# Performance work log

Measured on AMD Instinct MI355X. Metric: run time of the kernel, lower is better.

Reference implementation:

```python
import jax, jax.numpy as jnp
import numpy as np
import math

B, NX, NY = 8, 1024, 1024
DIM_X = DIM_Y = DIM = 1024
H = 8


def layer_norm(x, g, b, eps=1e-5):
    mu = jnp.mean(x, axis=-1, keepdims=True)
    var = jnp.mean(jnp.square(x - mu), axis=-1, keepdims=True)
    return (x - mu) * jax.lax.rsqrt(var + eps) * g + b


def setup_inputs() -> dict:
    key = jax.random.key(0)
    ks = jax.random.split(key, 12)
    s = 1.0 / math.sqrt(DIM)
    return {
        "X": jax.random.normal(ks[0], (B, NX, DIM_X), jnp.float32),
        "Y": jax.random.normal(ks[1], (B, NY, DIM_Y), jnp.float32),
        "mask": jax.random.bernoulli(ks[2], 0.1, (B, NY)),  # True = masked out
        "Wq": jax.random.normal(ks[3], (DIM_X, DIM), jnp.float32) * s,
        "bq": jnp.zeros((DIM,), jnp.float32),
        "Wk": jax.random.normal(ks[4], (DIM_Y, DIM), jnp.float32) * s,
        "bk": jnp.zeros((DIM,), jnp.float32),
        "Wv": jax.random.normal(ks[5], (DIM_Y, DIM), jnp.float32) * s,
        "bv": jnp.zeros((DIM,), jnp.float32),
        "Wo": jax.random.normal(ks[6], (DIM, DIM), jnp.float32) * s,
        "bo": jnp.zeros((DIM,), jnp.float32),
        "g1": jnp.ones((DIM,), jnp.float32),
        "b1": jnp.zeros((DIM,), jnp.float32),
        "g2": jnp.ones((DIM,), jnp.float32),
        "b2": jnp.zeros((DIM,), jnp.float32),
    }


def reference(X, Y, mask, Wq, bq, Wk, bk, Wv, bv, Wo, bo, g1, b1, g2, b2):
    Q = X @ Wq + bq            # [B, NX, DIM]
    K = Y @ Wk + bk            # [B, NY, DIM]
    V = Y @ Wv + bv            # [B, NY, DIM]
    Dh = DIM // H
    Qh = Q.reshape(B, NX, H, Dh)
    Kh = K.reshape(B, NY, H, Dh)
    Vh = V.reshape(B, NY, H, Dh)
    # NOTE: original scales by sqrt(dim) (full model dim), not sqrt(head_dim)
    logits = jnp.einsum("bqhd,bkhd->bhqk", Qh, Kh) / math.sqrt(DIM)
    logits = jnp.where(mask[:, None, None, :], -jnp.inf, logits)
    A = jax.nn.softmax(logits, axis=-1)
    A = jnp.where(jnp.isnan(A), 0.0, A)  # fully-masked rows -> 0
    attn = jnp.einsum("bhqk,bkhd->bqhd", A, Vh).reshape(B, NX, DIM)
    O = layer_norm(Q + attn, g1, b1)
    O = layer_norm(O + jax.nn.relu(O @ Wo + bo), g2, b2)
    return O
```

## Files before the change

### kernel.cpp

```cpp
#include <hip/hip_runtime.h>
#include <stdint.h>


typedef unsigned short u16;
typedef unsigned int u32;
typedef __attribute__((ext_vector_type(8))) short s16x8;
typedef __attribute__((ext_vector_type(4))) float f32x4;
typedef __attribute__((ext_vector_type(16))) float f32x16;
typedef __attribute__((ext_vector_type(4))) u16 u16x4;

typedef __attribute__((address_space(1))) const void* as1cv;
typedef __attribute__((address_space(3))) void* as3v;

#define DEVINL __device__ __forceinline__

DEVINL u16 f2bf(float f) {
  union { float f; u32 u; } v; v.f = f;
  return (u16)((v.u + 0x7FFFu + ((v.u >> 16) & 1u)) >> 16);
}
DEVINL float bf2f(u16 x) {
  union { u32 u; float f; } v; v.u = ((u32)x) << 16;
  return v.f;
}
DEVINL u32 cvtpk_bf16(float lo, float hi) {
  u32 r;
  asm("v_cvt_pk_bf16_f32 %0, %1, %2" : "=v"(r) : "v"(lo), "v"(hi));
  return r;
}
DEVINL float fexp2(float x) {
  float r;
  asm("v_exp_f32 %0, %1" : "=v"(r) : "v"(x));
  return r;
}
DEVINL void gload_lds16(const void* g, void* l) {
  __builtin_amdgcn_global_load_lds((as1cv)g, (as3v)l, 16, 0, 0);
}
DEVINL f32x4 mfma16(s16x8 a, s16x8 b, f32x4 c) {
  return __builtin_amdgcn_mfma_f32_16x16x32_bf16(a, b, c, 0, 0, 0);
}
DEVINL f32x16 mfma32(s16x8 a, s16x8 b, f32x16 c) {
  return __builtin_amdgcn_mfma_f32_32x32x16_bf16(a, b, c, 0, 0, 0);
}

__global__ __launch_bounds__(256) void prep_all(
    const float* __restrict__ X, u16* __restrict__ Xbf,
    const float* __restrict__ Y, u16* __restrict__ Ybf,
    const float* __restrict__ W0, const float* __restrict__ W1,
    const float* __restrict__ W2, const float* __restrict__ W3,
    u16* __restrict__ T0, u16* __restrict__ T1,
    u16* __restrict__ T2, u16* __restrict__ T3,
    const u32* __restrict__ mraw, float* __restrict__ maskb) {
  const int bid = blockIdx.x;
  const int t = threadIdx.x;
  if (bid < 16384) {
    int i = bid * 256 + t;
    const float* in = X;
    u16* out = Xbf;
    if (i >= 2097152) { i -= 2097152; in = Y; out = Ybf; }
    float4 v = *(const float4*)(in + (size_t)i * 4);
    u16x4 o; o[0] = f2bf(v.x); o[1] = f2bf(v.y); o[2] = f2bf(v.z); o[3] = f2bf(v.w);
    *(u16x4*)(out + (size_t)i * 4) = o;
    return;
  }
  if (bid < 20480) {
    const int r = bid - 16384;
    const int z = r >> 10, tile = r & 1023;
    const int bx = tile & 31, by = tile >> 5;
    const float* W = (z == 0) ? W0 : (z == 1) ? W1 : (z == 2) ? W2 : W3;
    u16* T = (z == 0) ? T0 : (z == 1) ? T1 : (z == 2) ? T2 : T3;
    __shared__ float tl[32][33];
    const int tx = t & 31, ty = t >> 5;
    const int N0 = bx << 5, K0 = by << 5;
#pragma unroll
    for (int i = 0; i < 4; ++i)
      tl[ty + i * 8][tx] = W[(size_t)(K0 + ty + i * 8) * 1024 + N0 + tx];
    __syncthreads();
#pragma unroll
    for (int i = 0; i < 4; ++i)
      T[(size_t)(N0 + ty + i * 8) * 1024 + K0 + tx] = f2bf(tl[tx][ty + i * 8]);
    return;
  }
  __shared__ int mode;
  int fB = 0, fF = 0;
  for (int i = t; i < 2048; i += 256) {
    u32 v = mraw[i];
    if (v == 0x3F800000u) fF = 1;
    else if (v > 1u) fB = 1;
  }
  if (t == 0) mode = 0;
  __syncthreads();
  if (fB) atomicOr(&mode, 1);
  if (fF) atomicOr(&mode, 2);
  __syncthreads();
  const int md = mode;
  const int idx = (bid - 20480) * 256 + t;
  int v;
  if (md & 1)       v = ((const unsigned char*)mraw)[idx] != 0;
  else if (md & 2)  v = ((const float*)mraw)[idx] != 0.0f;
  else              v = ((const int*)mraw)[idx] != 0;
  maskb[idx] = v ? -3e30f : -11.54156032f;
}

template <int MODE>
__global__ __launch_bounds__(256, 2) void gemm_nt(
    const u16* __restrict__ A, const u16* __restrict__ Bt,
    const float* __restrict__ bias, float* __restrict__ outF,
    u16* __restrict__ outBF, const u16* __restrict__ residBF) {
  __shared__ u16 lA[128 * 64];
  __shared__ u16 lB[128 * 64];

  const int id = blockIdx.x;
  const int cpx = gridDim.x >> 3;
  const int swz = (id & 7) * cpx + (id >> 3);
  const int mb = swz >> 3;
  const int nb = swz & 7;

  const int tid = threadIdx.x;
  const int w = tid >> 6, l = tid & 63;
  const int wm = w >> 1, wn = w & 1;
  const int lrow = l & 15, lk = l >> 4;

  const int sr = l >> 3;
  const int scol = ((l & 7) << 4) ^ (sr << 4);
  const char* gA = (const char*)A + (size_t)(mb * 128) * 2048;
  const char* gB = (const char*)Bt + (size_t)(nb * 128) * 2048;

  f32x4 acc[4][4];
#pragma unroll
  for (int i = 0; i < 4; ++i)
#pragma unroll
    for (int j = 0; j < 4; ++j) acc[i][j] = f32x4{0.f, 0.f, 0.f, 0.f};

  for (int kt = 0; kt < 16; ++kt) {
    const int kb = kt * 128;
#pragma unroll
    for (int c = 0; c < 4; ++c) {
      int row = (w * 4 + c) * 8 + sr;
      gload_lds16(gA + (size_t)row * 2048 + kb + scol, (char*)lA + (w * 4 + c) * 1024);
      gload_lds16(gB + (size_t)row * 2048 + kb + scol, (char*)lB + (w * 4 + c) * 1024);
    }
    __syncthreads();
#pragma unroll
    for (int kc = 0; kc < 2; ++kc) {
      s16x8 af[4], bfr[4];
#pragma unroll
      for (int mi = 0; mi < 4; ++mi) {
        int row = wm * 64 + mi * 16 + lrow;
        int off = row * 128 + ((lk * 16 + kc * 64) ^ ((row & 7) << 4));
        af[mi] = *(const s16x8*)((const char*)lA + off);
      }
#pragma unroll
      for (int ni = 0; ni < 4; ++ni) {
        int row = wn * 64 + ni * 16 + lrow;
        int off = row * 128 + ((lk * 16 + kc * 64) ^ ((row & 7) << 4));
        bfr[ni] = *(const s16x8*)((const char*)lB + off);
      }
      __builtin_amdgcn_s_setprio(1);
#pragma unroll
      for (int mi = 0; mi < 4; ++mi)
#pragma unroll
        for (int ni = 0; ni < 4; ++ni)
          acc[mi][ni] = mfma16(af[mi], bfr[ni], acc[mi][ni]);
      __builtin_amdgcn_s_setprio(0);
    }
    __syncthreads();
  }

  const int growb = mb * 128 + wm * 64;
  const int gcolb = nb * 128 + wn * 64;
  float bs[4];
#pragma unroll
  for (int ni = 0; ni < 4; ++ni) bs[ni] = bias[gcolb + ni * 16 + lrow];

#pragma unroll
  for (int mi = 0; mi < 4; ++mi) {
    const int grow0 = growb + mi * 16 + lk * 4;
#pragma unroll
    for (int ni = 0; ni < 4; ++ni) {
      const int gcol = gcolb + ni * 16 + lrow;
      if (MODE == 2) {
        u16x4 pk;
#pragma unroll
        for (int r = 0; r < 4; ++r) pk[r] = f2bf(acc[mi][ni][r] + bs[ni]);
        size_t flat = ((size_t)((grow0 >> 10) << 10) + gcol) * 1024 + (grow0 & 1023);
        *(u16x4*)(outBF + flat) = pk;
      } else {
#pragma unroll
        for (int r = 0; r < 4; ++r) {
          float v = acc[mi][ni][r] + bs[ni];
          size_t idx = (size_t)(grow0 + r) * 1024 + gcol;
          if (MODE == 1) { outBF[idx] = f2bf(v); }
          if (MODE == 3) { outBF[idx] = f2bf(bf2f(residBF[idx]) + fmaxf(v, 0.f)); }
        }
      }
    }
  }
}

__global__ __launch_bounds__(256, 2) void attn_fwd(
    const u16* __restrict__ Qbf, const u16* __restrict__ Kbf,
    const u16* __restrict__ Vt, const float* __restrict__ maskb,
    u16* __restrict__ attnO) {
  __shared__ u16 lK[2][64 * 128];
  __shared__ u16 lV[2][128 * 64];
  __shared__ float lM[1024];

  const int id = blockIdx.x;
  const int xcd = id & 7, seq = id >> 3;
  const int bh = xcd * 8 + (seq >> 3);
  const int qb = seq & 7;
  const int b = bh >> 3, h = bh & 7;
  const int tid = threadIdx.x;
  const int w = tid >> 6, l = tid & 63;
  const int q32 = l & 31, hi = l >> 5;

  const u16* Qrow = Qbf + ((size_t)(b * 1024 + qb * 128 + w * 32 + q32)) * 1024 + h * 128;
  s16x8 qf[8];
#pragma unroll
  for (int dc = 0; dc < 8; ++dc) qf[dc] = *(const s16x8*)(Qrow + dc * 16 + hi * 8);

  const int srK = l >> 4, slK = l & 15;
  int soK[4], soV[4];
#pragma unroll
  for (int c = 0; c < 4; ++c) {
    int rowK = (w * 4 + c) * 4 + srK;
    soK[c] = rowK * 2048 + ((slK << 4) ^ ((rowK & 15) << 4));
    int pairid = (w * 4 + c) * 4 + (l >> 4);
    int u = (l & 15) ^ (pairid & 15);
    int d = pairid * 2 + (u >> 3);
    soV[c] = d * 2048 + (u & 7) * 16;
  }
  const char* pgK = (const char*)(Kbf + ((size_t)(b * 1024)) * 1024 + h * 128);
  const char* pgV = (const char*)(Vt + ((size_t)(b * 1024 + h * 128)) * 1024);

  int loK[8], loV[4];
#pragma unroll
  for (int c = 0; c < 8; ++c)
    loK[c] = q32 * 256 + ((c * 32 + hi * 16) ^ ((q32 & 15) << 4));
#pragma unroll
  for (int c = 0; c < 4; ++c)
    loV[c] = (q32 >> 1) * 256 +
             (((((q32 & 1) << 3) | (c * 2 + hi)) ^ ((q32 >> 1) & 15)) << 4);

  if (w == 0) {
#pragma unroll
    for (int c = 0; c < 4; ++c)
      gload_lds16(maskb + b * 1024 + c * 256 + l * 4, (char*)lM + c * 1024);
  }

  float l_ = 0.f;
  f32x16 oacc[4];
#pragma unroll
  for (int i = 0; i < 4; ++i)
#pragma unroll
    for (int r = 0; r < 16; ++r) oacc[i][r] = 0.f;

  const float SCL = 0.04508422f;

#define ATT_STAGE(NXT, TN)                                                    \
  {                                                                           \
    const char* pk_ = pgK + (size_t)(TN)*131072;                              \
    const char* pv_ = pgV + (size_t)(TN)*128;                                 \
    _Pragma("unroll")                                                         \
    for (int c = 0; c < 4; ++c) {                                             \
      gload_lds16(pk_ + soK[c], (char*)lK[NXT] + w * 4096 + c * 1024);        \
      gload_lds16(pv_ + soV[c], (char*)lV[NXT] + w * 4096 + c * 1024);        \
    }                                                                         \
  }

#define ATT_COMPUTE(CUR, PMT)                                                 \
  {                                                                           \
    f32x16 sc[2];                                                             \
    _Pragma("unroll")                                                         \
    for (int kb = 0; kb < 2; ++kb)                                            \
      _Pragma("unroll")                                                       \
      for (int r = 0; r < 16; ++r) sc[kb][r] = 0.f;                           \
    __builtin_amdgcn_s_setprio(1);                                            \
    _Pragma("unroll")                                                         \
    for (int dc = 0; dc < 8; ++dc) {                                          \
      _Pragma("unroll")                                                       \
      for (int kb = 0; kb < 2; ++kb) {                                        \
        s16x8 kf = *(const s16x8*)((const char*)lK[CUR] + loK[dc] + kb * 8192); \
        sc[kb] = mfma32(kf, qf[dc], sc[kb]);                                  \
      }                                                                       \
    }                                                                         \
    __builtin_amdgcn_s_setprio(0);                                            \
    float rs = 0.f;                                                           \
    _Pragma("unroll")                                                         \
    for (int kb = 0; kb < 2; ++kb) {                                          \
      f32x4 mv[4];                                                            \
      _Pragma("unroll")                                                       \
      for (int g = 0; g < 4; ++g)                                             \
        mv[g] = *(const f32x4*)((PMT) + kb * 128 + g * 32);                   \
      _Pragma("unroll")                                                       \
      for (int r = 0; r < 16; ++r) {                                          \
        float pe = fexp2(fmaf(sc[kb][r], SCL, mv[r >> 2][r & 3]));            \
        sc[kb][r] = pe;                                                       \
        rs += pe;                                                             \
      }                                                                       \
    }                                                                         \
    rs += __shfl_xor(rs, 32);                                                 \
    l_ += rs;                                                                 \
    u32 pk[2][8];                                                             \
    _Pragma("unroll")                                                         \
    for (int kb = 0; kb < 2; ++kb)                                            \
      _Pragma("unroll")                                                       \
      for (int r2 = 0; r2 < 8; ++r2)                                          \
        pk[kb][r2] = cvtpk_bf16(sc[kb][2 * r2], sc[kb][2 * r2 + 1]);          \
    _Pragma("unroll")                                                         \
    for (int kc = 0; kc < 4; ++kc) {                                          \
      const int kb = kc >> 1;                                                 \
      const int ra = (kc & 1) * 4;                                            \
      u32 x0 = pk[kb][ra + 0], y0 = pk[kb][ra + 2];                           \
      u32 x1 = pk[kb][ra + 1], y1 = pk[kb][ra + 3];                           \
      asm("v_permlane32_swap_b32 %0, %1" : "+v"(x0), "+v"(y0));               \
      asm("v_permlane32_swap_b32 %0, %1" : "+v"(x1), "+v"(y1));               \
      union { u32 u[4]; s16x8 v; } pa;                                        \
      pa.u[0] = x0; pa.u[1] = x1; pa.u[2] = y0; pa.u[3] = y1;                 \
      __builtin_amdgcn_s_setprio(1);                                          \
      _Pragma("unroll")                                                       \
      for (int nb = 0; nb < 4; ++nb) {                                        \
        s16x8 vb = *(const s16x8*)((const char*)lV[CUR] + loV[kc] + nb * 4096); \
        oacc[nb] = mfma32(pa.v, vb, oacc[nb]);                                \
      }                                                                       \
      __builtin_amdgcn_s_setprio(0);                                          \
    }                                                                         \
  }

  const char* pM0 = (const char*)lM + hi * 16;

  ATT_STAGE(0, 0);
  __syncthreads();
  for (int it = 0; it < 7; ++it) {
    const char* pMa = pM0 + it * 512;
    ATT_STAGE(1, 2 * it + 1);
    ATT_COMPUTE(0, pMa);
    __syncthreads();
    ATT_STAGE(0, 2 * it + 2);
    ATT_COMPUTE(1, pMa + 256);
    __syncthreads();
  }
  {
    const char* pMa = pM0 + 7 * 512;
    ATT_STAGE(1, 15);
    ATT_COMPUTE(0, pMa);
    __syncthreads();
    ATT_COMPUTE(1, pMa + 256);
  }
#undef ATT_STAGE
#undef ATT_COMPUTE

  float inv = (l_ > 1e-20f) ? (1.0f / l_) : 0.f;
  u16* obase = attnO + ((size_t)(b * 1024 + qb * 128 + w * 32)) * 1024 + h * 128;
#pragma unroll
  for (int r = 0; r < 16; ++r) {
    int qr = (r & 3) + 8 * (r >> 2) + 4 * hi;
    float iv = __shfl(inv, qr);
#pragma unroll
    for (int nb = 0; nb < 4; ++nb)
      obase[(size_t)qr * 1024 + nb * 32 + q32] = f2bf(oacc[nb][r] * iv);
  }
}

__global__ __launch_bounds__(256) void ln_fused(
    const float* __restrict__ aF, const u16* __restrict__ aBF,
    const u16* __restrict__ baddBF, const float* __restrict__ g,
    const float* __restrict__ bt, float* __restrict__ outF,
    u16* __restrict__ outBF) {
  const int row = blockIdx.x;
  const int c = threadIdx.x << 2;
  const size_t base = (size_t)row * 1024 + c;
  float4 h;
  if (aF) {
    h = *(const float4*)(aF + base);
  } else {
    u16x4 u = *(const u16x4*)(aBF + base);
    h.x = bf2f(u[0]); h.y = bf2f(u[1]); h.z = bf2f(u[2]); h.w = bf2f(u[3]);
  }
  if (baddBF) {
    u16x4 u = *(const u16x4*)(baddBF + base);
    h.x += bf2f(u[0]); h.y += bf2f(u[1]); h.z += bf2f(u[2]); h.w += bf2f(u[3]);
  }
  float s = (h.x + h.y) + (h.z + h.w);
  float q = (h.x * h.x + h.y * h.y) + (h.z * h.z + h.w * h.w);
#pragma unroll
  for (int msk = 1; msk < 64; msk <<= 1) {
    s += __shfl_xor(s, msk);
    q += __shfl_xor(q, msk);
  }
  __shared__ float sh[8];
  const int w = threadIdx.x >> 6;
  if ((threadIdx.x & 63) == 0) { sh[w] = s; sh[4 + w] = q; }
  __syncthreads();
  s = (sh[0] + sh[1]) + (sh[2] + sh[3]);
  q = (sh[4] + sh[5]) + (sh[6] + sh[7]);
  const float mu = s * (1.f / 1024.f);
  const float var = q * (1.f / 1024.f) - mu * mu;
  const float rstd = rsqrtf(var + 1e-5f);
  const float4 gv = *(const float4*)(g + c);
  const float4 bv = *(const float4*)(bt + c);
  float4 o;
  o.x = (h.x - mu) * rstd * gv.x + bv.x;
  o.y = (h.y - mu) * rstd * gv.y + bv.y;
  o.z = (h.z - mu) * rstd * gv.z + bv.z;
  o.w = (h.w - mu) * rstd * gv.w + bv.w;
  if (outF) *(float4*)(outF + base) = o;
  if (outBF) {
    u16x4 ub; ub[0] = f2bf(o.x); ub[1] = f2bf(o.y); ub[2] = f2bf(o.z); ub[3] = f2bf(o.w);
    *(u16x4*)(outBF + base) = ub;
  }
}

extern "C" void kernel_launch(void* const* d_in, const int* in_sizes, int n_in,
                              void* d_out, int out_size, void* d_ws, size_t ws_size,
                              hipStream_t stream) {
  const float* X  = (const float*)d_in[0];
  const float* Y  = (const float*)d_in[1];
  const void*  mask = d_in[2];
  const float* Wq = (const float*)d_in[3];
  const float* bq = (const float*)d_in[4];
  const float* Wk = (const float*)d_in[5];
  const float* bk = (const float*)d_in[6];
  const float* Wv = (const float*)d_in[7];
  const float* bv = (const float*)d_in[8];
  const float* Wo = (const float*)d_in[9];
  const float* bo = (const float*)d_in[10];
  const float* g1 = (const float*)d_in[11];
  const float* b1 = (const float*)d_in[12];
  const float* g2 = (const float*)d_in[13];
  const float* b2 = (const float*)d_in[14];
  float* out = (float*)d_out;

  char* ws = (char*)d_ws;
  const size_t MB = 1024ull * 1024ull;
  u16* Xbf    = (u16*)(ws + 0);
  u16* Ybf    = (u16*)(ws + 16 * MB);
  u16* Qbf    = (u16*)(ws + 32 * MB);
  u16* Kbf    = (u16*)(ws + 48 * MB);
  u16* Vt     = (u16*)(ws + 64 * MB);
  u16* attnbf = (u16*)(ws + 80 * MB);
  u16* Wqt = (u16*)(ws + 112 * MB);
  u16* Wkt = (u16*)(ws + 114 * MB);
  u16* Wvt = (u16*)(ws + 116 * MB);
  u16* Wot = (u16*)(ws + 118 * MB);
  float* maskb = (float*)(ws + 120 * MB);
  u16* Rbf = Kbf;
  u16* O1bf = Xbf;

  prep_all<<<dim3(20512), dim3(256), 0, stream>>>(
      X, Xbf, Y, Ybf, Wq, Wk, Wv, Wo, Wqt, Wkt, Wvt, Wot,
      (const u32*)mask, maskb);

  gemm_nt<1><<<dim3(512), dim3(256), 0, stream>>>(Xbf, Wqt, bq, nullptr, Qbf, nullptr);
  gemm_nt<1><<<dim3(512), dim3(256), 0, stream>>>(Ybf, Wkt, bk, nullptr, Kbf, nullptr);
  gemm_nt<2><<<dim3(512), dim3(256), 0, stream>>>(Ybf, Wvt, bv, nullptr, Vt, nullptr);

  attn_fwd<<<dim3(512), dim3(256), 0, stream>>>(Qbf, Kbf, Vt, maskb, attnbf);

  ln_fused<<<dim3(8192), dim3(256), 0, stream>>>(nullptr, Qbf, attnbf, g1, b1, nullptr, O1bf);
  gemm_nt<3><<<dim3(512), dim3(256), 0, stream>>>(O1bf, Wot, bo, nullptr, Rbf, O1bf);
  ln_fused<<<dim3(8192), dim3(256), 0, stream>>>(nullptr, Rbf, nullptr, g2, b2, out, nullptr);
}
```

Before: 178.5 us.

## Merge QKV GEMMs into one launch and restructure GEMM and attention pipelining

Replaces the three separate Q/K/V projection launches with a single 1536-block kernel that picks its operands by block group. The GEMM k-loop now issues the next tile's global-to-LDS loads right after the fragment reads, overlapping them with the second half of the MFMAs, where before every load sat behind a barrier. Attention shrinks V to a single buffer, stages K and V separately with explicit vmcnt waits and raw barriers, and computes LDS offsets inline to save registers. The goal is to cut launch overhead, fill the GPU better and hide load latency, at the cost of more fragile hand-placed synchronisation.

Result: faster. 170.0 us (-4.8%).

```diff
diff --git a/kernel.cpp b/kernel.cpp
--- a/kernel.cpp
+++ b/kernel.cpp
@@ -40,6 +40,19 @@
 }
 DEVINL f32x16 mfma32(s16x8 a, s16x8 b, f32x16 c) {
   return __builtin_amdgcn_mfma_f32_32x32x16_bf16(a, b, c, 0, 0, 0);
+}
+template <int N> DEVINL void wait_vm() {
+  asm volatile("s_waitcnt vmcnt(%0)" :: "i"(N) : "memory");
+  __builtin_amdgcn_sched_barrier(0);
+}
+DEVINL void wait_lgkm0() {
+  asm volatile("s_waitcnt lgkmcnt(0)" ::: "memory");
+  __builtin_amdgcn_sched_barrier(0);
+}
+DEVINL void barrier_raw() {
+  __builtin_amdgcn_sched_barrier(0);
+  __builtin_amdgcn_s_barrier();
+  __builtin_amdgcn_sched_barrier(0);
 }
 
 __global__ __launch_bounds__(256) void prep_all(
@@ -101,25 +114,93 @@
   maskb[idx] = v ? -3e30f : -11.54156032f;
 }
 
-template <int MODE>
-__global__ __launch_bounds__(256, 2) void gemm_nt(
-    const u16* __restrict__ A, const u16* __restrict__ Bt,
-    const float* __restrict__ bias, float* __restrict__ outF,
-    u16* __restrict__ outBF, const u16* __restrict__ residBF) {
+#define GEMM_KLOOP                                                            \
+  for (int kt = 0; kt < 16; ++kt) {                                           \
+    s16x8 af0[4], bf0[4], af1[4], bf1[4];                                     \
+    _Pragma("unroll")                                                         \
+    for (int mi = 0; mi < 4; ++mi) {                                          \
+      int row = wm * 64 + mi * 16 + lrow;                                     \
+      int off = row * 128 + ((lk * 16) ^ ((row & 7) << 4));                   \
+      af0[mi] = *(const s16x8*)((const char*)lA + off);                       \
+    }                                                                         \
+    _Pragma("unroll")                                                         \
+    for (int ni = 0; ni < 4; ++ni) {                                          \
+      int row = wn * 64 + ni * 16 + lrow;                                     \
+      int off = row * 128 + ((lk * 16) ^ ((row & 7) << 4));                   \
+      bf0[ni] = *(const s16x8*)((const char*)lB + off);                       \
+    }                                                                         \
+    _Pragma("unroll")                                                         \
+    for (int mi = 0; mi < 4; ++mi)                                            \
+      _Pragma("unroll")                                                       \
+      for (int ni = 0; ni < 4; ++ni)                                          \
+        acc[mi][ni] = mfma16(af0[mi], bf0[ni], acc[mi][ni]);                  \
+    _Pragma("unroll")                                                         \
+    for (int mi = 0; mi < 4; ++mi) {                                          \
+      int row = wm * 64 + mi * 16 + lrow;                                     \
+      int off = row * 128 + ((lk * 16 + 64) ^ ((row & 7) << 4));              \
+      af1[mi] = *(const s16x8*)((const char*)lA + off);                       \
+    }                                                                         \
+    _Pragma("unroll")                                                         \
+    for (int ni = 0; ni < 4; ++ni) {                                          \
+      int row = wn * 64 + ni * 16 + lrow;                                     \
+      int off = row * 128 + ((lk * 16 + 64) ^ ((row & 7) << 4));              \
+      bf1[ni] = *(const s16x8*)((const char*)lB + off);                       \
+    }                                                                         \
+    wait_lgkm0();                                                             \
+    barrier_raw();                                                            \
+    if (kt < 15) {                                                            \
+      const int kb = (kt + 1) * 128;                                          \
+      _Pragma("unroll")                                                       \
+      for (int c = 0; c < 4; ++c) {                                           \
+        int row = (w * 4 + c) * 8 + sr;                                       \
+        gload_lds16(gA + (size_t)row * 2048 + kb + scol,                      \
+                    (char*)lA + (w * 4 + c) * 1024);                          \
+        gload_lds16(gB + (size_t)row * 2048 + kb + scol,                      \
+                    (char*)lB + (w * 4 + c) * 1024);                          \
+      }                                                                       \
+    }                                                                         \
+    _Pragma("unroll")                                                         \
+    for (int mi = 0; mi < 4; ++mi)                                            \
+      _Pragma("unroll")                                                       \
+      for (int ni = 0; ni < 4; ++ni)                                          \
+        acc[mi][ni] = mfma16(af1[mi], bf1[ni], acc[mi][ni]);                  \
+    __syncthreads();                                                          \
+  }
+
+#define GEMM_PROLOGUE                                                         \
+  _Pragma("unroll")                                                           \
+  for (int c = 0; c < 4; ++c) {                                               \
+    int row = (w * 4 + c) * 8 + sr;                                           \
+    gload_lds16(gA + (size_t)row * 2048 + scol, (char*)lA + (w * 4 + c) * 1024); \
+    gload_lds16(gB + (size_t)row * 2048 + scol, (char*)lB + (w * 4 + c) * 1024); \
+  }                                                                           \
+  __syncthreads();
+
+__global__ __launch_bounds__(256, 2) void gemm_qkv(
+    const u16* __restrict__ Xbf, const u16* __restrict__ Ybf,
+    const u16* __restrict__ Wqt, const u16* __restrict__ Wkt,
+    const u16* __restrict__ Wvt,
+    const float* __restrict__ bq, const float* __restrict__ bk,
+    const float* __restrict__ bv,
+    u16* __restrict__ Qbf, u16* __restrict__ Kbf, u16* __restrict__ Vt) {
   __shared__ u16 lA[128 * 64];
   __shared__ u16 lB[128 * 64];
 
   const int id = blockIdx.x;
-  const int cpx = gridDim.x >> 3;
-  const int swz = (id & 7) * cpx + (id >> 3);
+  const int g = id >> 9;
+  const int sub = id & 511;
+  const int swz = (sub & 7) * 64 + (sub >> 3);
   const int mb = swz >> 3;
   const int nb = swz & 7;
+
+  const u16* A    = (g == 0) ? Xbf : Ybf;
+  const u16* Bt   = (g == 0) ? Wqt : (g == 1) ? Wkt : Wvt;
+  const float* bias = (g == 0) ? bq : (g == 1) ? bk : bv;
 
   const int tid = threadIdx.x;
   const int w = tid >> 6, l = tid & 63;
   const int wm = w >> 1, wn = w & 1;
   const int lrow = l & 15, lk = l >> 4;
-
   const int sr = l >> 3;
   const int scol = ((l & 7) << 4) ^ (sr << 4);
   const char* gA = (const char*)A + (size_t)(mb * 128) * 2048;
@@ -131,40 +212,8 @@
 #pragma unroll
     for (int j = 0; j < 4; ++j) acc[i][j] = f32x4{0.f, 0.f, 0.f, 0.f};
 
-  for (int kt = 0; kt < 16; ++kt) {
-    const int kb = kt * 128;
-#pragma unroll
-    for (int c = 0; c < 4; ++c) {
-      int row = (w * 4 + c) * 8 + sr;
-      gload_lds16(gA + (size_t)row * 2048 + kb + scol, (char*)lA + (w * 4 + c) * 1024);
-      gload_lds16(gB + (size_t)row * 2048 + kb + scol, (char*)lB + (w * 4 + c) * 1024);
-    }
-    __syncthreads();
-#pragma unroll
-    for (int kc = 0; kc < 2; ++kc) {
-      s16x8 af[4], bfr[4];
-#pragma unroll
-      for (int mi = 0; mi < 4; ++mi) {
-        int row = wm * 64 + mi * 16 + lrow;
-        int off = row * 128 + ((lk * 16 + kc * 64) ^ ((row & 7) << 4));
-        af[mi] = *(const s16x8*)((const char*)lA + off);
-      }
-#pragma unroll
-      for (int ni = 0; ni < 4; ++ni) {
-        int row = wn * 64 + ni * 16 + lrow;
-        int off = row * 128 + ((lk * 16 + kc * 64) ^ ((row & 7) << 4));
-        bfr[ni] = *(const s16x8*)((const char*)lB + off);
-      }
-      __builtin_amdgcn_s_setprio(1);
-#pragma unroll
-      for (int mi = 0; mi < 4; ++mi)
-#pragma unroll
-        for (int ni = 0; ni < 4; ++ni)
-          acc[mi][ni] = mfma16(af[mi], bfr[ni], acc[mi][ni]);
-      __builtin_amdgcn_s_setprio(0);
-    }
-    __syncthreads();
-  }
+  GEMM_PROLOGUE
+  GEMM_KLOOP
 
   const int growb = mb * 128 + wm * 64;
   const int gcolb = nb * 128 + wn * 64;
@@ -172,26 +221,83 @@
 #pragma unroll
   for (int ni = 0; ni < 4; ++ni) bs[ni] = bias[gcolb + ni * 16 + lrow];
 
+  if (g == 2) {
+#pragma unroll
+    for (int mi = 0; mi < 4; ++mi) {
+      const int grow0 = growb + mi * 16 + lk * 4;
+#pragma unroll
+      for (int ni = 0; ni < 4; ++ni) {
+        const int gcol = gcolb + ni * 16 + lrow;
+        u16x4 pk;
+#pragma unroll
+        for (int r = 0; r < 4; ++r) pk[r] = f2bf(acc[mi][ni][r] + bs[ni]);
+        size_t flat = ((size_t)((grow0 >> 10) << 10) + gcol) * 1024 + (grow0 & 1023);
+        *(u16x4*)(Vt + flat) = pk;
+      }
+    }
+  } else {
+    u16* outBF = g ? Kbf : Qbf;
+#pragma unroll
+    for (int mi = 0; mi < 4; ++mi) {
+      const int grow0 = growb + mi * 16 + lk * 4;
+#pragma unroll
+      for (int ni = 0; ni < 4; ++ni) {
+        const int gcol = gcolb + ni * 16 + lrow;
+#pragma unroll
+        for (int r = 0; r < 4; ++r)
+          outBF[(size_t)(grow0 + r) * 1024 + gcol] = f2bf(acc[mi][ni][r] + bs[ni]);
+      }
+    }
+  }
+}
+
+__global__ __launch_bounds__(256, 2) void gemm_o(
+    const u16* __restrict__ A, const u16* __restrict__ Bt,
+    const float* __restrict__ bias, u16* __restrict__ outBF,
+    const u16* __restrict__ residBF) {
+  __shared__ u16 lA[128 * 64];
+  __shared__ u16 lB[128 * 64];
+
+  const int id = blockIdx.x;
+  const int swz = (id & 7) * 64 + (id >> 3);
+  const int mb = swz >> 3;
+  const int nb = swz & 7;
+
+  const int tid = threadIdx.x;
+  const int w = tid >> 6, l = tid & 63;
+  const int wm = w >> 1, wn = w & 1;
+  const int lrow = l & 15, lk = l >> 4;
+  const int sr = l >> 3;
+  const int scol = ((l & 7) << 4) ^ (sr << 4);
+  const char* gA = (const char*)A + (size_t)(mb * 128) * 2048;
+  const char* gB = (const char*)Bt + (size_t)(nb * 128) * 2048;
+
+  f32x4 acc[4][4];
+#pragma unroll
+  for (int i = 0; i < 4; ++i)
+#pragma unroll
+    for (int j = 0; j < 4; ++j) acc[i][j] = f32x4{0.f, 0.f, 0.f, 0.f};
+
+  GEMM_PROLOGUE
+  GEMM_KLOOP
+
+  const int growb = mb * 128 + wm * 64;
+  const int gcolb = nb * 128 + wn * 64;
+  float bs[4];
+#pragma unroll
+  for (int ni = 0; ni < 4; ++ni) bs[ni] = bias[gcolb + ni * 16 + lrow];
+
 #pragma unroll
   for (int mi = 0; mi < 4; ++mi) {
     const int grow0 = growb + mi * 16 + lk * 4;
 #pragma unroll
     for (int ni = 0; ni < 4; ++ni) {
       const int gcol = gcolb + ni * 16 + lrow;
-      if (MODE == 2) {
-        u16x4 pk;
-#pragma unroll
-        for (int r = 0; r < 4; ++r) pk[r] = f2bf(acc[mi][ni][r] + bs[ni]);
-        size_t flat = ((size_t)((grow0 >> 10) << 10) + gcol) * 1024 + (grow0 & 1023);
-        *(u16x4*)(outBF + flat) = pk;
-      } else {
-#pragma unroll
-        for (int r = 0; r < 4; ++r) {
-          float v = acc[mi][ni][r] + bs[ni];
-          size_t idx = (size_t)(grow0 + r) * 1024 + gcol;
-          if (MODE == 1) { outBF[idx] = f2bf(v); }
-          if (MODE == 3) { outBF[idx] = f2bf(bf2f(residBF[idx]) + fmaxf(v, 0.f)); }
-        }
+#pragma unroll
+      for (int r = 0; r < 4; ++r) {
+        float v = acc[mi][ni][r] + bs[ni];
+        size_t idx = (size_t)(grow0 + r) * 1024 + gcol;
+        outBF[idx] = f2bf(bf2f(residBF[idx]) + fmaxf(v, 0.f));
       }
     }
   }
@@ -202,7 +308,7 @@
     const u16* __restrict__ Vt, const float* __restrict__ maskb,
     u16* __restrict__ attnO) {
   __shared__ u16 lK[2][64 * 128];
-  __shared__ u16 lV[2][128 * 64];
+  __shared__ u16 lV[128 * 64];
   __shared__ float lM[1024];
 
   const int id = blockIdx.x;
@@ -233,10 +339,10 @@
   const char* pgK = (const char*)(Kbf + ((size_t)(b * 1024)) * 1024 + h * 128);
   const char* pgV = (const char*)(Vt + ((size_t)(b * 1024 + h * 128)) * 1024);
 
-  int loK[8], loV[4];
-#pragma unroll
-  for (int c = 0; c < 8; ++c)
-    loK[c] = q32 * 256 + ((c * 32 + hi * 16) ^ ((q32 & 15) << 4));
+  const int bK = q32 * 256;
+  const int swzK = (q32 & 15) << 4;
+  const int hib = hi * 16;
+  int loV[4];
 #pragma unroll
   for (int c = 0; c < 4; ++c)
     loV[c] = (q32 >> 1) * 256 +
@@ -247,6 +353,9 @@
     for (int c = 0; c < 4; ++c)
       gload_lds16(maskb + b * 1024 + c * 256 + l * 4, (char*)lM + c * 1024);
   }
+#pragma unroll
+  for (int c = 0; c < 4; ++c)
+    gload_lds16(pgK + soK[c], (char*)lK[0] + w * 4096 + c * 1024);
 
   float l_ = 0.f;
   f32x16 oacc[4];
@@ -256,20 +365,27 @@
     for (int r = 0; r < 16; ++r) oacc[i][r] = 0.f;
 
   const float SCL = 0.04508422f;
-
-#define ATT_STAGE(NXT, TN)                                                    \
+  const char* pM0 = (const char*)lM + hi * 16;
+
+#define STAGE_K(TN, BUF)                                                      \
   {                                                                           \
     const char* pk_ = pgK + (size_t)(TN)*131072;                              \
+    _Pragma("unroll")                                                         \
+    for (int c = 0; c < 4; ++c)                                               \
+      gload_lds16(pk_ + soK[c], (char*)lK[BUF] + w * 4096 + c * 1024);        \
+  }
+#define STAGE_V(TN)                                                           \
+  {                                                                           \
     const char* pv_ = pgV + (size_t)(TN)*128;                                 \
     _Pragma("unroll")                                                         \
-    for (int c = 0; c < 4; ++c) {                                             \
-      gload_lds16(pk_ + soK[c], (char*)lK[NXT] + w * 4096 + c * 1024);        \
-      gload_lds16(pv_ + soV[c], (char*)lV[NXT] + w * 4096 + c * 1024);        \
-    }                                                                         \
-  }
-
-#define ATT_COMPUTE(CUR, PMT)                                                 \
+    for (int c = 0; c < 4; ++c)                                               \
+      gload_lds16(pv_ + soV[c], (char*)lV + w * 4096 + c * 1024);             \
+  }
+
+#define ATT_TILE(T, CUR, FIRST, LAST)                                         \
   {                                                                           \
+    STAGE_V(T);                                                               \
+    if (FIRST) { wait_vm<4>(); barrier_raw(); }                               \
     f32x16 sc[2];                                                             \
     _Pragma("unroll")                                                         \
     for (int kb = 0; kb < 2; ++kb)                                            \
@@ -278,20 +394,22 @@
     __builtin_amdgcn_s_setprio(1);                                            \
     _Pragma("unroll")                                                         \
     for (int dc = 0; dc < 8; ++dc) {                                          \
+      int offk = bK + (((dc * 32) | hib) ^ swzK);                             \
       _Pragma("unroll")                                                       \
       for (int kb = 0; kb < 2; ++kb) {                                        \
-        s16x8 kf = *(const s16x8*)((const char*)lK[CUR] + loK[dc] + kb * 8192); \
+        s16x8 kf = *(const s16x8*)((const char*)lK[CUR] + offk + kb * 8192);  \
         sc[kb] = mfma32(kf, qf[dc], sc[kb]);                                  \
       }                                                                       \
     }                                                                         \
     __builtin_amdgcn_s_setprio(0);                                            \
+    const char* pMa = pM0 + (T)*256;                                          \
     float rs = 0.f;                                                           \
     _Pragma("unroll")                                                         \
     for (int kb = 0; kb < 2; ++kb) {                                          \
       f32x4 mv[4];                                                            \
       _Pragma("unroll")                                                       \
       for (int g = 0; g < 4; ++g)                                             \
-        mv[g] = *(const f32x4*)((PMT) + kb * 128 + g * 32);                   \
+        mv[g] = *(const f32x4*)(pMa + kb * 128 + g * 32);                     \
       _Pragma("unroll")                                                       \
       for (int r = 0; r < 16; ++r) {                                          \
         float pe = fexp2(fmaf(sc[kb][r], SCL, mv[r >> 2][r & 3]));            \
@@ -301,18 +419,17 @@
     }                                                                         \
     rs += __shfl_xor(rs, 32);                                                 \
     l_ += rs;                                                                 \
-    u32 pk[2][8];                                                             \
-    _Pragma("unroll")                                                         \
-    for (int kb = 0; kb < 2; ++kb)                                            \
-      _Pragma("unroll")                                                       \
-      for (int r2 = 0; r2 < 8; ++r2)                                          \
-        pk[kb][r2] = cvtpk_bf16(sc[kb][2 * r2], sc[kb][2 * r2 + 1]);          \
+    if (!(LAST)) STAGE_K((T) + 1, (CUR) ^ 1);                                 \
+    if (LAST) wait_vm<0>(); else wait_vm<4>();                                \
+    barrier_raw();                                                            \
     _Pragma("unroll")                                                         \
     for (int kc = 0; kc < 4; ++kc) {                                          \
       const int kb = kc >> 1;                                                 \
-      const int ra = (kc & 1) * 4;                                            \
-      u32 x0 = pk[kb][ra + 0], y0 = pk[kb][ra + 2];                           \
-      u32 x1 = pk[kb][ra + 1], y1 = pk[kb][ra + 3];                           \
+      const int ra2 = (kc & 1) * 8;                                           \
+      u32 x0 = cvtpk_bf16(sc[kb][ra2 + 0], sc[kb][ra2 + 1]);                  \
+      u32 x1 = cvtpk_bf16(sc[kb][ra2 + 2], sc[kb][ra2 + 3]);                  \
+      u32 y0 = cvtpk_bf16(sc[kb][ra2 + 4], sc[kb][ra2 + 5]);                  \
+      u32 y1 = cvtpk_bf16(sc[kb][ra2 + 6], sc[kb][ra2 + 7]);                  \
       asm("v_permlane32_swap_b32 %0, %1" : "+v"(x0), "+v"(y0));               \
       asm("v_permlane32_swap_b32 %0, %1" : "+v"(x1), "+v"(y1));               \
       union { u32 u[4]; s16x8 v; } pa;                                        \
@@ -320,35 +437,23 @@
       __builtin_amdgcn_s_setprio(1);                                          \
       _Pragma("unroll")                                                       \
       for (int nb = 0; nb < 4; ++nb) {                                        \
-        s16x8 vb = *(const s16x8*)((const char*)lV[CUR] + loV[kc] + nb * 4096); \
+        s16x8 vb = *(const s16x8*)((const char*)lV + loV[kc] + nb * 4096);    \
         oacc[nb] = mfma32(pa.v, vb, oacc[nb]);                                \
       }                                                                       \
       __builtin_amdgcn_s_setprio(0);                                          \
     }                                                                         \
-  }
-
-  const char* pM0 = (const char*)lM + hi * 16;
-
-  ATT_STAGE(0, 0);
-  __syncthreads();
+    if (!(LAST)) { wait_vm<0>(); barrier_raw(); }                             \
+  }
+
+  ATT_TILE(0, 0, true, false);
   for (int it = 0; it < 7; ++it) {
-    const char* pMa = pM0 + it * 512;
-    ATT_STAGE(1, 2 * it + 1);
-    ATT_COMPUTE(0, pMa);
-    __syncthreads();
-    ATT_STAGE(0, 2 * it + 2);
-    ATT_COMPUTE(1, pMa + 256);
-    __syncthreads();
-  }
-  {
-    const char* pMa = pM0 + 7 * 512;
-    ATT_STAGE(1, 15);
-    ATT_COMPUTE(0, pMa);
-    __syncthreads();
-    ATT_COMPUTE(1, pMa + 256);
-  }
-#undef ATT_STAGE
-#undef ATT_COMPUTE
+    ATT_TILE(2 * it + 1, 1, false, false);
+    ATT_TILE(2 * it + 2, 0, false, false);
+  }
+  ATT_TILE(15, 1, false, true);
+#undef ATT_TILE
+#undef STAGE_K
+#undef STAGE_V
 
   float inv = (l_ > 1e-20f) ? (1.0f / l_) : 0.f;
   u16* obase = attnO + ((size_t)(b * 1024 + qb * 128 + w * 32)) * 1024 + h * 128;
@@ -451,13 +556,12 @@
       X, Xbf, Y, Ybf, Wq, Wk, Wv, Wo, Wqt, Wkt, Wvt, Wot,
       (const u32*)mask, maskb);
 
-  gemm_nt<1><<<dim3(512), dim3(256), 0, stream>>>(Xbf, Wqt, bq, nullptr, Qbf, nullptr);
-  gemm_nt<1><<<dim3(512), dim3(256), 0, stream>>>(Ybf, Wkt, bk, nullptr, Kbf, nullptr);
-  gemm_nt<2><<<dim3(512), dim3(256), 0, stream>>>(Ybf, Wvt, bv, nullptr, Vt, nullptr);
+  gemm_qkv<<<dim3(1536), dim3(256), 0, stream>>>(
+      Xbf, Ybf, Wqt, Wkt, Wvt, bq, bk, bv, Qbf, Kbf, Vt);
 
   attn_fwd<<<dim3(512), dim3(256), 0, stream>>>(Qbf, Kbf, Vt, maskb, attnbf);
 
   ln_fused<<<dim3(8192), dim3(256), 0, stream>>>(nullptr, Qbf, attnbf, g1, b1, nullptr, O1bf);
-  gemm_nt<3><<<dim3(512), dim3(256), 0, stream>>>(O1bf, Wot, bo, nullptr, Rbf, O1bf);
+  gemm_o<<<dim3(512), dim3(256), 0, stream>>>(O1bf, Wot, bo, Rbf, O1bf);
   ln_fused<<<dim3(8192), dim3(256), 0, stream>>>(nullptr, Rbf, nullptr, g2, b2, out, nullptr);
 }
```
